# Kernel optimization log

Measured on AMD Instinct MI355X. Metric: run time of the kernel, lower is better.

## Reference

```python
import math
import jax, jax.numpy as jnp
import numpy as np

N_EXPERTS = 8
TOP_K = 2
CAP_FACTOR = 1.25

def _capacity(num_tokens: int) -> int:
    cap = math.floor(TOP_K * CAP_FACTOR * num_tokens / N_EXPERTS)
    cap += cap % 2
    return max(int(cap), 2)

def setup_inputs() -> dict:
    key = jax.random.key(0)
    k1, k2 = jax.random.split(key)
    x = jax.random.normal(k1, (2, 2048, 1024), dtype=jnp.float32)
    w_gate = jax.random.normal(k2, (N_EXPERTS, 1024), dtype=jnp.float32) * 0.02
    return {"x": x, "w_gate": w_gate}

def reference(x, w_gate):
    B, S, D = x.shape
    N = B * S
    E, K = N_EXPERTS, TOP_K
    cap = _capacity(N)

    xf = x.astype(jnp.float32)
    router_logits = jnp.einsum('bsd,ed->bse', xf, w_gate)  # [B,S,E]
    lf = router_logits.reshape(N, E)

    # top-k gating: softmax over only the top-k logits (others -inf)
    topv, topi = jax.lax.top_k(lf, K)                       # [N,K]
    masked = jnp.full((N, E), -jnp.inf, dtype=lf.dtype)
    masked = masked.at[jnp.arange(N)[:, None], topi].set(topv)
    router_probs = jax.nn.softmax(masked, axis=-1)          # [N,E]

    # per-(k,token) expert one-hot, ranked by global cumsum order (k-major)
    mask = jax.nn.one_hot(topi, E, dtype=jnp.int32)         # [N,K,E]
    mask = jnp.transpose(mask, (1, 0, 2))                   # [K,N,E]
    rank = jnp.cumsum(mask.reshape(K * N, E), axis=0) - 1   # position within each expert
    rank = rank.reshape(K, N, E)
    mask = mask * (rank < cap)                              # drop tokens over capacity
    rank_k = jnp.sum(mask * rank, axis=-1)                  # [K,N] slot index per assignment

    weights = mask.astype(router_probs.dtype) * router_probs[None]   # [K,N,E]
    rank_oh = jax.nn.one_hot(rank_k, cap, dtype=router_probs.dtype)  # [K,N,cap]
    # sum over k of outer(weights[k,n,:], rank_oh[k,n,:]) -> [N,E,cap]
    expert_weights = jnp.einsum('kne,knc->nec', weights, rank_oh)
    expert_mask = expert_weights > 0                        # [N,E,cap] bool

    x_flat = x.reshape(N, D)
    # gather token features into expert batches: [E,cap,N] @ [N,D]
    expert_batches = jnp.einsum('nec,nd->ecd', expert_mask.astype(x.dtype), x_flat)

    return expert_weights, expert_mask, expert_batches, router_logits
```

## Files before the change

### kernel.cpp

```cpp
#include <hip/hip_runtime.h>
#include <hip/hip_bf16.h>
#include <math.h>

#define DIM 1024
#define NEXP 8

__global__ __launch_bounds__(256) void k_router(
    const float* __restrict__ x, const float* __restrict__ wg,
    float* __restrict__ logits,
    int* __restrict__ e1, int* __restrict__ e2,
    float* __restrict__ p1, float* __restrict__ p2, int N)
{
    __shared__ float wlds[NEXP * DIM];
    const int tid = threadIdx.x;
    for (int i = tid; i < NEXP * DIM; i += 256) wlds[i] = wg[i];
    __syncthreads();

    const int wave = tid >> 6, lane = tid & 63;

    for (int t = 0; t < 4; ++t) {
        const int n = blockIdx.x * 16 + wave * 4 + t;
        if (n >= N) return;

        const float4* x4 = (const float4*)x + (size_t)n * (DIM / 4);
        float s[NEXP];
#pragma unroll
        for (int e = 0; e < NEXP; ++e) s[e] = 0.0f;

#pragma unroll
        for (int i = 0; i < 4; ++i) {
            const int idx = lane + 64 * i;
            const float4 v = x4[idx];
#pragma unroll
            for (int e = 0; e < NEXP; ++e) {
                const float* wrow = &wlds[e * DIM + idx * 4];
                float acc = s[e];
                acc = fmaf(v.x, wrow[0], acc);
                acc = fmaf(v.y, wrow[1], acc);
                acc = fmaf(v.z, wrow[2], acc);
                acc = fmaf(v.w, wrow[3], acc);
                s[e] = acc;
            }
        }

#pragma unroll
        for (int off = 32; off >= 1; off >>= 1) {
#pragma unroll
            for (int e = 0; e < NEXP; ++e) s[e] += __shfl_xor(s[e], off, 64);
        }

        int be1 = 0; float bv1 = s[0];
#pragma unroll
        for (int e = 1; e < NEXP; ++e) { if (s[e] > bv1) { bv1 = s[e]; be1 = e; } }
        int be2 = -1; float bv2 = -INFINITY;
#pragma unroll
        for (int e = 0; e < NEXP; ++e) { if (e != be1 && s[e] > bv2) { bv2 = s[e]; be2 = e; } }

        const float tt = expf(bv2 - bv1);
        const float inv = 1.0f / (1.0f + tt);

        if (lane == 0) {
#pragma unroll
            for (int e = 0; e < NEXP; ++e) logits[(size_t)n * NEXP + e] = s[e];
            e1[n] = be1; e2[n] = be2;
            p1[n] = inv; p2[n] = tt * inv;
        }
    }
}

__global__ __launch_bounds__(1024) void k_scan(
    const int* __restrict__ e1, const int* __restrict__ e2,
    const float* __restrict__ p1, const float* __restrict__ p2,
    int* __restrict__ r1, int* __restrict__ r2,
    int* __restrict__ slot_token, int N, int cap)
{
    __shared__ unsigned long long emask[128 * NEXP];
    __shared__ int pre[128 * NEXP];

    const int tid = threadIdx.x;
    const int wave = tid >> 6, lane = tid & 63;
    const int cpk = N / 64;
    const int nchunks = 2 * cpk;
    const int nelem = nchunks * NEXP;

    for (int i = tid; i < NEXP * cap; i += 1024) slot_token[i] = -1;

    for (int c = wave; c < nchunks; c += 16) {
        const int k = c / cpk, r = c % cpk;
        const int n = r * 64 + lane;
        const int e = (k == 0 ? e1 : e2)[n];
#pragma unroll
        for (int q = 0; q < NEXP; ++q) {
            const unsigned long long b = __ballot(e == q);
            if (lane == q) emask[c * NEXP + q] = b;
        }
    }
    __syncthreads();

    if (tid < nelem) pre[tid] = (int)__popcll(emask[tid]);
    __syncthreads();
    for (int off = NEXP; off < nelem; off <<= 1) {
        int add = 0;
        if (tid < nelem && tid >= off) add = pre[tid - off];
        __syncthreads();
        if (tid < nelem) pre[tid] += add;
        __syncthreads();
    }

    const unsigned long long below =
        (lane == 0) ? 0ULL : ((~0ULL) >> (64 - lane));
    for (int c = wave; c < nchunks; c += 16) {
        const int k = c / cpk, r = c % cpk;
        const int n = r * 64 + lane;
        const float p = (k == 0 ? p1 : p2)[n];
        int e = 0; unsigned long long mm = 0;
#pragma unroll
        for (int q = 0; q < NEXP; ++q) {
            const unsigned long long b = emask[c * NEXP + q];
            if ((b >> lane) & 1ULL) { e = q; mm = b; }
        }
        const int bexc = (c > 0) ? pre[(c - 1) * NEXP + e] : 0;
        const int rank = bexc + (int)__popcll(mm & below);
        int* rout = (k == 0 ? r1 : r2);
        if (rank < cap) {
            rout[n] = rank;
            slot_token[(size_t)e * cap + rank] = (p > 0.0f) ? n : -1;
        } else {
            rout[n] = -1;
        }
    }
}

__global__ __launch_bounds__(256) void k_fill(
    const int* __restrict__ e1, const int* __restrict__ e2,
    const float* __restrict__ p1, const float* __restrict__ p2,
    const int* __restrict__ r1, const int* __restrict__ r2,
    const int* __restrict__ slot_token, const float* __restrict__ x,
    float* __restrict__ W, float* __restrict__ M, float* __restrict__ Bt,
    int cap, int N, int nrows)
{
    const int wave = threadIdx.x >> 6, lane = threadIdx.x & 63;
    const int row = blockIdx.x * 4 + wave;
    if (row >= nrows) return;

    const int nwm = N * NEXP;
    if (row < nwm) {
        const int n = row >> 3, e = row & 7;
        float p = 0.0f; int r = -1;
        if (e == e1[n])      { r = r1[n]; p = p1[n]; }
        else if (e == e2[n]) { r = r2[n]; p = p2[n]; }
        const bool on = (r >= 0);

        float4* Wr = (float4*)(W + (size_t)row * cap);
        float4* Mr = (float4*)(M + (size_t)row * cap);
        const int nf4 = cap >> 2;
        const float mval = (p > 0.0f) ? 1.0f : 0.0f;
        for (int c4 = lane; c4 < nf4; c4 += 64) {
            const int c = c4 * 4;
            float4 w = make_float4(0.f, 0.f, 0.f, 0.f);
            float4 m = make_float4(0.f, 0.f, 0.f, 0.f);
            if (on) {
                const int d = r - c;
                if (d == 0)      { w.x = p; m.x = mval; }
                else if (d == 1) { w.y = p; m.y = mval; }
                else if (d == 2) { w.z = p; m.z = mval; }
                else if (d == 3) { w.w = p; m.w = mval; }
            }
            Wr[c4] = w; Mr[c4] = m;
        }
    } else {
        const int brow = row - nwm;
        const int tok = slot_token[brow];
        float4* out = (float4*)(Bt + (size_t)brow * DIM);
        if (tok >= 0) {
            const float4* src = (const float4*)(x + (size_t)tok * DIM);
#pragma unroll
            for (int i = 0; i < 4; ++i) out[lane + 64 * i] = src[lane + 64 * i];
        } else {
            const float4 z = make_float4(0.f, 0.f, 0.f, 0.f);
#pragma unroll
            for (int i = 0; i < 4; ++i) out[lane + 64 * i] = z;
        }
    }
}

extern "C" void kernel_launch(void* const* d_in, const int* in_sizes, int n_in,
                              void* d_out, int out_size, void* d_ws, size_t ws_size,
                              hipStream_t stream)
{
    const float* x  = (const float*)d_in[0];
    const float* wg = (const float*)d_in[1];

    const int N = in_sizes[0] / DIM;
    int cap = (5 * N) / 16;
    cap += cap & 1;
    if (cap < 2) cap = 2;

    const size_t szW = (size_t)N * NEXP * cap;
    float* W  = (float*)d_out;
    float* M  = W + szW;
    float* Bt = M + szW;
    float* L  = Bt + (size_t)NEXP * cap * DIM;

    char* w = (char*)d_ws;
    int*   e1 = (int*)w;        w += (size_t)N * sizeof(int);
    int*   e2 = (int*)w;        w += (size_t)N * sizeof(int);
    float* p1 = (float*)w;      w += (size_t)N * sizeof(float);
    float* p2 = (float*)w;      w += (size_t)N * sizeof(float);
    int*   r1 = (int*)w;        w += (size_t)N * sizeof(int);
    int*   r2 = (int*)w;        w += (size_t)N * sizeof(int);
    int*   slot_token = (int*)w;

    k_router<<<(N + 15) / 16, 256, 0, stream>>>(x, wg, L, e1, e2, p1, p2, N);
    k_scan<<<1, 1024, 0, stream>>>(e1, e2, p1, p2, r1, r2, slot_token, N, cap);
    const int nrows = N * NEXP + NEXP * cap;
    k_fill<<<(nrows + 3) / 4, 256, 0, stream>>>(e1, e2, p1, p2, r1, r2,
                                                slot_token, x, W, M, Bt,
                                                cap, N, nrows);
}
```

Baseline: 406.6 us.

## Zero W/M with bulk kernel and scatter nonzeros from scan

Replaces the per-row fill of the dense weight and mask outputs with a grid-stride non-temporal zeroing kernel, then has the scan kernel scatter the single nonzero entry per assignment directly. The gather kernel now only handles expert batches and uses non-temporal stores. This removes the rank workspace and the per-row branching and index reads in the fill. The trade-off is that the scattered writes must be ordered after the zeroing, which holds only because both kernels run on the same stream.

```diff
diff --git a/kernel.cpp b/kernel.cpp
--- a/kernel.cpp
+++ b/kernel.cpp
@@ -4,6 +4,18 @@
 
 #define DIM 1024
 #define NEXP 8
+
+typedef float fv4 __attribute__((ext_vector_type(4)));
+
+__global__ __launch_bounds__(256) void k_zero(fv4* __restrict__ dst,
+                                              size_t n4)
+{
+    const fv4 z = {0.f, 0.f, 0.f, 0.f};
+    size_t i = (size_t)blockIdx.x * 256 + threadIdx.x;
+    const size_t stride = (size_t)gridDim.x * 256;
+    for (; i < n4; i += stride)
+        __builtin_nontemporal_store(z, &dst[i]);
+}
 
 __global__ __launch_bounds__(256) void k_router(
     const float* __restrict__ x, const float* __restrict__ wg,
@@ -71,7 +83,7 @@
 __global__ __launch_bounds__(1024) void k_scan(
     const int* __restrict__ e1, const int* __restrict__ e2,
     const float* __restrict__ p1, const float* __restrict__ p2,
-    int* __restrict__ r1, int* __restrict__ r2,
+    float* __restrict__ W, float* __restrict__ M,
     int* __restrict__ slot_token, int N, int cap)
 {
     __shared__ unsigned long long emask[128 * NEXP];
@@ -121,66 +133,35 @@
         }
         const int bexc = (c > 0) ? pre[(c - 1) * NEXP + e] : 0;
         const int rank = bexc + (int)__popcll(mm & below);
-        int* rout = (k == 0 ? r1 : r2);
         if (rank < cap) {
-            rout[n] = rank;
+            const size_t off = ((size_t)n * NEXP + e) * cap + rank;
+            W[off] = p;
+            M[off] = (p > 0.0f) ? 1.0f : 0.0f;
             slot_token[(size_t)e * cap + rank] = (p > 0.0f) ? n : -1;
-        } else {
-            rout[n] = -1;
-        }
-    }
-}
-
-__global__ __launch_bounds__(256) void k_fill(
-    const int* __restrict__ e1, const int* __restrict__ e2,
-    const float* __restrict__ p1, const float* __restrict__ p2,
-    const int* __restrict__ r1, const int* __restrict__ r2,
+        }
+    }
+}
+
+__global__ __launch_bounds__(256) void k_batches(
     const int* __restrict__ slot_token, const float* __restrict__ x,
-    float* __restrict__ W, float* __restrict__ M, float* __restrict__ Bt,
-    int cap, int N, int nrows)
+    float* __restrict__ Bt, int nrows)
 {
     const int wave = threadIdx.x >> 6, lane = threadIdx.x & 63;
     const int row = blockIdx.x * 4 + wave;
     if (row >= nrows) return;
 
-    const int nwm = N * NEXP;
-    if (row < nwm) {
-        const int n = row >> 3, e = row & 7;
-        float p = 0.0f; int r = -1;
-        if (e == e1[n])      { r = r1[n]; p = p1[n]; }
-        else if (e == e2[n]) { r = r2[n]; p = p2[n]; }
-        const bool on = (r >= 0);
-
-        float4* Wr = (float4*)(W + (size_t)row * cap);
-        float4* Mr = (float4*)(M + (size_t)row * cap);
-        const int nf4 = cap >> 2;
-        const float mval = (p > 0.0f) ? 1.0f : 0.0f;
-        for (int c4 = lane; c4 < nf4; c4 += 64) {
-            const int c = c4 * 4;
-            float4 w = make_float4(0.f, 0.f, 0.f, 0.f);
-            float4 m = make_float4(0.f, 0.f, 0.f, 0.f);
-            if (on) {
-                const int d = r - c;
-                if (d == 0)      { w.x = p; m.x = mval; }
-                else if (d == 1) { w.y = p; m.y = mval; }
-                else if (d == 2) { w.z = p; m.z = mval; }
-                else if (d == 3) { w.w = p; m.w = mval; }
-            }
-            Wr[c4] = w; Mr[c4] = m;
-        }
+    const int tok = slot_token[row];
+    fv4* out = (fv4*)(Bt + (size_t)row * DIM);
+    if (tok >= 0) {
+        const fv4* src = (const fv4*)(x + (size_t)tok * DIM);
+#pragma unroll
+        for (int i = 0; i < 4; ++i)
+            __builtin_nontemporal_store(src[lane + 64 * i], &out[lane + 64 * i]);
     } else {
-        const int brow = row - nwm;
-        const int tok = slot_token[brow];
-        float4* out = (float4*)(Bt + (size_t)brow * DIM);
-        if (tok >= 0) {
-            const float4* src = (const float4*)(x + (size_t)tok * DIM);
-#pragma unroll
-            for (int i = 0; i < 4; ++i) out[lane + 64 * i] = src[lane + 64 * i];
-        } else {
-            const float4 z = make_float4(0.f, 0.f, 0.f, 0.f);
-#pragma unroll
-            for (int i = 0; i < 4; ++i) out[lane + 64 * i] = z;
-        }
+        const fv4 z = {0.f, 0.f, 0.f, 0.f};
+#pragma unroll
+        for (int i = 0; i < 4; ++i)
+            __builtin_nontemporal_store(z, &out[lane + 64 * i]);
     }
 }
 
@@ -207,14 +188,14 @@
     int*   e2 = (int*)w;        w += (size_t)N * sizeof(int);
     float* p1 = (float*)w;      w += (size_t)N * sizeof(float);
     float* p2 = (float*)w;      w += (size_t)N * sizeof(float);
-    int*   r1 = (int*)w;        w += (size_t)N * sizeof(int);
-    int*   r2 = (int*)w;        w += (size_t)N * sizeof(int);
     int*   slot_token = (int*)w;
 
+    const size_t n4 = (2 * szW) / 4;
+    k_zero<<<4096, 256, 0, stream>>>((fv4*)W, n4);
+
     k_router<<<(N + 15) / 16, 256, 0, stream>>>(x, wg, L, e1, e2, p1, p2, N);
-    k_scan<<<1, 1024, 0, stream>>>(e1, e2, p1, p2, r1, r2, slot_token, N, cap);
-    const int nrows = N * NEXP + NEXP * cap;
-    k_fill<<<(nrows + 3) / 4, 256, 0, stream>>>(e1, e2, p1, p2, r1, r2,
-                                                slot_token, x, W, M, Bt,
-                                                cap, N, nrows);
-}
+    k_scan<<<1, 1024, 0, stream>>>(e1, e2, p1, p2, W, M, slot_token, N, cap);
+
+    const int nrows_b = NEXP * cap;
+    k_batches<<<(nrows_b + 3) / 4, 256, 0, stream>>>(slot_token, x, Bt, nrows_b);
+}
```

Result: slower. 430.6 us (+5.9%).
